# Performance work log

Hardware: AMD Instinct MI355X
Metric: run time of the kernel (lower is better)

Reference implementation:

```python
import jax, jax.numpy as jnp
import numpy as np

TEMP = 0.07
LAMBDA_INFONCE = 1.0
LAMBDA_NTXENT = 0.5
EPS = 1e-8

B, S, H, C = 32, 2048, 1024, 5


def _l2norm(x):
    # F.normalize-style row L2 normalization
    n = jnp.sqrt(jnp.sum(x * x, axis=1, keepdims=True))
    return x / jnp.maximum(n, 1e-12)


def _proj(x, W1, b1, W2, b2):
    h = jax.nn.relu(x @ W1 + b1)
    return _l2norm(h @ W2 + b2)


def setup_inputs() -> dict:
    key = jax.random.key(0)
    ks = jax.random.split(key, 12)
    sc1 = 1.0 / np.sqrt(H)
    sc2 = 1.0 / np.sqrt(H // 2)
    sc3 = 1.0 / np.sqrt(2 * H)
    return {
        "span_features": jax.random.normal(ks[0], (B, S, H), jnp.float32),
        "aspect_logits": jax.random.normal(ks[1], (B, S, C), jnp.float32),
        "opinion_logits": jax.random.normal(ks[2], (B, S, C), jnp.float32),
        "sentiment_labels": jax.random.randint(ks[3], (B,), 0, 3),
        "Wa1": jax.random.normal(ks[4], (H, H // 2), jnp.float32) * sc1,
        "ba1": jnp.zeros((H // 2,), jnp.float32),
        "Wa2": jax.random.normal(ks[5], (H // 2, 128), jnp.float32) * sc2,
        "ba2": jnp.zeros((128,), jnp.float32),
        "Wo1": jax.random.normal(ks[6], (H, H // 2), jnp.float32) * sc1,
        "bo1": jnp.zeros((H // 2,), jnp.float32),
        "Wo2": jax.random.normal(ks[7], (H // 2, 128), jnp.float32) * sc2,
        "bo2": jnp.zeros((128,), jnp.float32),
        "Ws1": jax.random.normal(ks[8], (2 * H, H), jnp.float32) * sc3,
        "bs1": jnp.zeros((H,), jnp.float32),
        "Ws2": jax.random.normal(ks[9], (H, 256), jnp.float32) * sc1,
        "bs2": jnp.zeros((256,), jnp.float32),
    }


def _pool(span_features, logits):
    # attention pooling: softmax over seq of summed non-O class logits
    w = jax.nn.softmax(logits[:, :, 1:].sum(axis=-1), axis=-1)  # [B, S]
    return jnp.einsum("bsh,bs->bh", span_features, w)  # [B, H]


def _infonce(a, o, labels):
    n = a.shape[0]
    sim = (a @ o.T) / TEMP  # [B, B]
    same = labels[:, None] == labels[None, :]
    eye = jnp.eye(n, dtype=a.dtype)
    pos_mask = eye + 0.5 * (same & (eye == 0)).astype(a.dtype)
    exp_sim = jnp.exp(sim)
    return -jnp.mean(jnp.log((exp_sim * pos_mask).sum(1) / exp_sim.sum(1) + EPS))


def _ntxent(s, labels):
    n = s.shape[0]
    s = _l2norm(s)
    sim = (s @ s.T) / TEMP
    same = (labels[:, None] == labels[None, :]).astype(s.dtype)
    mask = same - jnp.eye(n, dtype=s.dtype)
    exp_sim = jnp.exp(sim)
    pos = (exp_sim * mask).sum(1)
    neg = (exp_sim * (1.0 - mask)).sum(1)
    pos_count = mask.sum(1)
    has_pos = pos_count > 0
    row = jnp.where(has_pos,
                    -jnp.log(pos / (pos + neg) + EPS) / jnp.maximum(pos_count, 1.0),
                    0.0)
    return row.sum() / jnp.maximum(has_pos.sum(), 1).astype(s.dtype)


def reference(span_features, aspect_logits, opinion_logits, sentiment_labels,
              Wa1, ba1, Wa2, ba2, Wo1, bo1, Wo2, bo2, Ws1, bs1, Ws2, bs2):
    a_emb = _pool(span_features, aspect_logits)   # [B, H]
    o_emb = _pool(span_features, opinion_logits)  # [B, H]
    a_proj = _proj(a_emb, Wa1, ba1, Wa2, ba2)     # [B, 128]
    o_proj = _proj(o_emb, Wo1, bo1, Wo2, bo2)     # [B, 128]
    infonce = _infonce(a_proj, o_proj, sentiment_labels)
    s_proj = _proj(jnp.concatenate([a_emb, o_emb], axis=-1), Ws1, bs1, Ws2, bs2)
    ntxent = _ntxent(s_proj, sentiment_labels)
    # generation_embeddings is None -> cross_modal_loss = 0
    return LAMBDA_INFONCE * infonce + LAMBDA_NTXENT * ntxent
```

## Files before the change

kernel.cpp:

```cpp
#include <hip/hip_runtime.h>
#include <hip/hip_bf16.h>

#define BB 32
#define SS 2048
#define HH 1024
#define CC 5
#define TEMP_INV (1.0f/0.07f)

__global__ __launch_bounds__(256) void pool_weights(const float* __restrict__ alog,
                             const float* __restrict__ olog,
                             float* __restrict__ w_a,
                             float* __restrict__ w_o) {
    int b = blockIdx.x >> 1;
    int which = blockIdx.x & 1;
    const float* lg = which ? olog : alog;
    float* wout = which ? w_o : w_a;
    __shared__ float raw[SS * CC];
    __shared__ float sl[SS];
    __shared__ float red[256];
    int t = threadIdx.x;
    const float4* src = (const float4*)(lg + (size_t)b * SS * CC);
    float4* dst = (float4*)raw;
    #pragma unroll 4
    for (int i = t; i < SS * CC / 4; i += 256) dst[i] = src[i];
    __syncthreads();
    for (int s = t; s < SS; s += 256) {
        int base = s * 5;
        sl[s] = raw[base + 1] + raw[base + 2] + raw[base + 3] + raw[base + 4];
    }
    __syncthreads();
    float m = -1e30f;
    for (int s = t; s < SS; s += 256) m = fmaxf(m, sl[s]);
    red[t] = m;
    __syncthreads();
    for (int o = 128; o > 0; o >>= 1) {
        if (t < o) red[t] = fmaxf(red[t], red[t + o]);
        __syncthreads();
    }
    m = red[0];
    __syncthreads();
    float sum = 0.f;
    for (int s = t; s < SS; s += 256) {
        float e = expf(sl[s] - m);
        sl[s] = e;
        sum += e;
    }
    red[t] = sum;
    __syncthreads();
    for (int o = 128; o > 0; o >>= 1) {
        if (t < o) red[t] += red[t + o];
        __syncthreads();
    }
    float inv = 1.0f / red[0];
    for (int s = t; s < SS; s += 256) wout[(size_t)b * SS + s] = sl[s] * inv;
}

__global__ __launch_bounds__(256) void pool_partial(const float* __restrict__ span,
                             const float* __restrict__ w_a,
                             const float* __restrict__ w_o,
                             float* __restrict__ part_a,
                             float* __restrict__ part_o) {
    int b = blockIdx.x >> 5;
    int chunk = blockIdx.x & 31;
    int t = threadIdx.x;
    __shared__ float wa[64], wo[64];
    int s0 = chunk * 64;
    if (t < 64) {
        wa[t] = w_a[(size_t)b * SS + s0 + t];
        wo[t] = w_o[(size_t)b * SS + s0 + t];
    }
    __syncthreads();
    const float4* sp = (const float4*)span + ((size_t)b * SS + s0) * (HH / 4) + t;
    float4 aa = {0.f, 0.f, 0.f, 0.f};
    float4 oo = {0.f, 0.f, 0.f, 0.f};
    #pragma unroll 8
    for (int ss = 0; ss < 64; ++ss) {
        float4 v = sp[(size_t)ss * (HH / 4)];
        float fa = wa[ss], fo = wo[ss];
        aa.x += v.x * fa; aa.y += v.y * fa; aa.z += v.z * fa; aa.w += v.w * fa;
        oo.x += v.x * fo; oo.y += v.y * fo; oo.z += v.z * fo; oo.w += v.w * fo;
    }
    size_t idx = ((size_t)chunk * BB + b) * HH + (size_t)t * 4;
    *(float4*)(part_a + idx) = aa;
    *(float4*)(part_o + idx) = oo;
}

__global__ __launch_bounds__(256) void pool_reduce(const float* __restrict__ part_a,
                            const float* __restrict__ part_o,
                            float* __restrict__ a_emb,
                            float* __restrict__ o_emb) {
    int gid = blockIdx.x * 256 + threadIdx.x;
    int which = gid >> 15;
    int r = gid & 32767;
    const float* p = which ? part_o : part_a;
    float s = 0.f;
    #pragma unroll
    for (int c = 0; c < 32; ++c) s += p[(size_t)c * 32768 + r];
    (which ? o_emb : a_emb)[r] = s;
}

__global__ __launch_bounds__(512) void gemm1_all(const float* __restrict__ a_emb, const float* __restrict__ o_emb,
                          const float* __restrict__ Wa1, const float* __restrict__ Wo1,
                          const float* __restrict__ Ws1,
                          float* __restrict__ p1_a, float* __restrict__ p1_o,
                          float* __restrict__ p1_s) {
    int bid = blockIdx.x;
    const float* xp; const float* W; float* part; int N, kb, jb;
    if (bid < 64) {
        jb = bid & 7; kb = bid >> 3; N = 512; W = Wa1; part = p1_a;
        xp = a_emb + kb * 128;
    } else if (bid < 128) {
        int r = bid - 64;
        jb = r & 7; kb = r >> 3; N = 512; W = Wo1; part = p1_o;
        xp = o_emb + kb * 128;
    } else {
        int r = bid - 128;
        jb = r & 15; kb = r >> 4; N = 1024; W = Ws1; part = p1_s;
        int kk0 = kb * 128;
        xp = (kk0 < 1024) ? (a_emb + kk0) : (o_emb + (kk0 - 1024));
    }
    int k0 = kb * 128;
    __shared__ float xs[32][128];
    int t = threadIdx.x;
    #pragma unroll
    for (int i = 0; i < 2; ++i) {
        int f = t + i * 512;
        int b = f >> 5;
        int kk = (f & 31) * 4;
        *(float4*)(&xs[b][kk]) = *(const float4*)(xp + (size_t)b * HH + kk);
    }
    __syncthreads();
    int jl = t & 63, bg = t >> 6;
    int j = jb * 64 + jl;
    float acc[4] = {0.f, 0.f, 0.f, 0.f};
    const float* Wp = W + (size_t)k0 * N + j;
    #pragma unroll 4
    for (int k = 0; k < 128; k += 4) {
        float w0 = Wp[(size_t)(k + 0) * N];
        float w1 = Wp[(size_t)(k + 1) * N];
        float w2 = Wp[(size_t)(k + 2) * N];
        float w3 = Wp[(size_t)(k + 3) * N];
        #pragma unroll
        for (int bi = 0; bi < 4; ++bi) {
            float4 xv = *(const float4*)(&xs[bg * 4 + bi][k]);
            acc[bi] += xv.x * w0 + xv.y * w1 + xv.z * w2 + xv.w * w3;
        }
    }
    float* pp = part + (size_t)kb * 32 * N + j;
    #pragma unroll
    for (int bi = 0; bi < 4; ++bi)
        pp[(size_t)(bg * 4 + bi) * N] = acc[bi];
}

__global__ __launch_bounds__(512) void layer2_all(const float* __restrict__ p1_a, const float* __restrict__ ba1,
                           const float* __restrict__ Wa2, const float* __restrict__ ba2,
                           const float* __restrict__ p1_o, const float* __restrict__ bo1,
                           const float* __restrict__ Wo2, const float* __restrict__ bo2,
                           const float* __restrict__ p1_s, const float* __restrict__ bs1,
                           const float* __restrict__ Ws2, const float* __restrict__ bs2,
                           float* __restrict__ a_proj, float* __restrict__ o_proj,
                           float* __restrict__ s_proj) {
    __shared__ float x[1024];
    __shared__ float red[512];
    int bid = blockIdx.x;
    int t = threadIdx.x;
    if (bid < 64) {
        int which = bid >> 5;
        int b = bid & 31;
        const float* part = which ? p1_o : p1_a;
        const float* b1 = which ? bo1 : ba1;
        const float* W2 = which ? Wo2 : Wa2;
        const float* b2 = which ? bo2 : ba2;
        float* out = (which ? o_proj : a_proj) + (size_t)b * 128;
        {
            float s = b1[t];
            #pragma unroll
            for (int kb = 0; kb < 8; ++kb) s += part[(size_t)kb * 32 * 512 + (size_t)b * 512 + t];
            x[t] = fmaxf(s, 0.f);
        }
        __syncthreads();
        int jj = t & 127, kh = t >> 7;
        int kbase = kh * 128;
        const float* Wc = W2 + (size_t)kbase * 128 + jj;
        float acc = 0.f;
        #pragma unroll 16
        for (int kk = 0; kk < 128; ++kk)
            acc += x[kbase + kk] * Wc[(size_t)kk * 128];
        if (kh == 0) acc += b2[jj];
        red[t] = acc;
        __syncthreads();
        float tot = 0.f;
        if (t < 128) tot = red[t] + red[t + 128] + red[t + 256] + red[t + 384];
        __syncthreads();
        if (t < 128) red[t] = tot * tot;
        __syncthreads();
        for (int o = 64; o > 0; o >>= 1) {
            if (t < o) red[t] += red[t + o];
            __syncthreads();
        }
        float n = fmaxf(sqrtf(red[0]), 1e-12f);
        if (t < 128) out[t] = tot / n;
    } else {
        int b = bid - 64;
        for (int j = t; j < 1024; j += 512) {
            float s = bs1[j];
            #pragma unroll
            for (int kb = 0; kb < 16; ++kb) s += p1_s[(size_t)kb * 32 * 1024 + (size_t)b * 1024 + j];
            x[j] = fmaxf(s, 0.f);
        }
        __syncthreads();
        int jj = t & 255, kh = t >> 8;
        int kbase = kh * 512;
        const float* Wc = Ws2 + (size_t)kbase * 256 + jj;
        float acc = 0.f;
        #pragma unroll 16
        for (int kk = 0; kk < 512; ++kk)
            acc += x[kbase + kk] * Wc[(size_t)kk * 256];
        if (kh == 0) acc += bs2[jj];
        red[t] = acc;
        __syncthreads();
        float tot = 0.f;
        if (t < 256) tot = red[t] + red[t + 256];
        __syncthreads();
        if (t < 256) red[t] = tot * tot;
        __syncthreads();
        for (int o = 128; o > 0; o >>= 1) {
            if (t < o) red[t] += red[t + o];
            __syncthreads();
        }
        float n = fmaxf(sqrtf(red[0]), 1e-12f);
        if (t < 256) s_proj[(size_t)b * 256 + t] = tot / n;
    }
}

__global__ __launch_bounds__(1024) void loss_kernel(const float* __restrict__ a_proj,
                            const float* __restrict__ o_proj,
                            const float* __restrict__ s_proj,
                            const int* __restrict__ labels,
                            float* __restrict__ out) {
    __shared__ float ap[BB][129];
    __shared__ float op[BB][129];
    __shared__ float sp[BB][257];
    __shared__ float rowv[BB], rownt[BB];
    __shared__ int hp[BB], lab[BB];
    int t = threadIdx.x;
    for (int idx = t; idx < BB * 128; idx += 1024) {
        int r = idx >> 7, c = idx & 127;
        ap[r][c] = a_proj[idx];
        op[r][c] = o_proj[idx];
    }
    for (int idx = t; idx < BB * 256; idx += 1024) {
        int r = idx >> 8, c = idx & 255;
        sp[r][c] = s_proj[idx];
    }
    if (t < BB) lab[t] = labels[t];
    __syncthreads();
    int i = t >> 5, j = t & 31;

    float ssq = 0.f;
    #pragma unroll
    for (int k = 0; k < 8; ++k) {
        float v = sp[i][j * 8 + k];
        ssq += v * v;
    }
    for (int m = 16; m > 0; m >>= 1) ssq += __shfl_xor(ssq, m, 64);
    float inv = 1.0f / fmaxf(sqrtf(ssq), 1e-12f);
    for (int k = j; k < 256; k += 32) sp[i][k] *= inv;
    __syncthreads();

    float dot = 0.f;
    #pragma unroll 16
    for (int k = 0; k < 128; ++k) dot += ap[i][k] * op[j][k];
    float e = expf(dot * TEMP_INV);
    float maskv = (i == j) ? 1.0f : ((lab[i] == lab[j]) ? 0.5f : 0.0f);
    float num = e * maskv, den = e;
    for (int m = 16; m > 0; m >>= 1) {
        num += __shfl_xor(num, m, 64);
        den += __shfl_xor(den, m, 64);
    }

    float dn = 0.f;
    #pragma unroll 16
    for (int k = 0; k < 256; ++k) dn += sp[i][k] * sp[j][k];
    float en = expf(dn * TEMP_INV);
    float mnt = (lab[i] == lab[j]) ? ((i == j) ? 0.f : 1.f) : 0.f;
    float pos = en * mnt, neg = en * (1.f - mnt), pc = mnt;
    for (int m = 16; m > 0; m >>= 1) {
        pos += __shfl_xor(pos, m, 64);
        neg += __shfl_xor(neg, m, 64);
        pc += __shfl_xor(pc, m, 64);
    }

    if (j == 0) {
        rowv[i] = -logf(num / den + 1e-8f);
        bool has = pc > 0.f;
        rownt[i] = has ? (-logf(pos / (pos + neg) + 1e-8f) / fmaxf(pc, 1.0f)) : 0.f;
        hp[i] = has ? 1 : 0;
    }
    __syncthreads();
    if (t == 0) {
        float inf = 0.f, nt = 0.f;
        int h = 0;
        for (int q = 0; q < BB; ++q) { inf += rowv[q]; nt += rownt[q]; h += hp[q]; }
        inf /= (float)BB;
        nt /= (float)(h > 0 ? h : 1);
        out[0] = 1.0f * inf + 0.5f * nt;
    }
}

extern "C" void kernel_launch(void* const* d_in, const int* in_sizes, int n_in,
                              void* d_out, int out_size, void* d_ws, size_t ws_size,
                              hipStream_t stream) {
    const float* span  = (const float*)d_in[0];
    const float* alog  = (const float*)d_in[1];
    const float* olog  = (const float*)d_in[2];
    const int*   labs  = (const int*)d_in[3];
    const float* Wa1   = (const float*)d_in[4];
    const float* ba1   = (const float*)d_in[5];
    const float* Wa2   = (const float*)d_in[6];
    const float* ba2   = (const float*)d_in[7];
    const float* Wo1   = (const float*)d_in[8];
    const float* bo1   = (const float*)d_in[9];
    const float* Wo2   = (const float*)d_in[10];
    const float* bo2   = (const float*)d_in[11];
    const float* Ws1   = (const float*)d_in[12];
    const float* bs1   = (const float*)d_in[13];
    const float* Ws2   = (const float*)d_in[14];
    const float* bs2   = (const float*)d_in[15];

    float* ws = (float*)d_ws;
    float* w_a    = ws;
    float* w_o    = ws + 65536;
    float* part_a = ws + 131072;
    float* part_o = ws + 1179648;
    float* a_emb  = ws + 2228224;
    float* o_emb  = ws + 2260992;
    float* p1_a   = ws + 2293760;
    float* p1_o   = ws + 2424832;
    float* p1_s   = ws + 2555904;
    float* a_proj = ws + 3080192;
    float* o_proj = ws + 3084288;
    float* s_proj = ws + 3088384;

    hipLaunchKernelGGL(pool_weights, dim3(64), dim3(256), 0, stream, alog, olog, w_a, w_o);
    hipLaunchKernelGGL(pool_partial, dim3(1024), dim3(256), 0, stream,
                       span, w_a, w_o, part_a, part_o);
    hipLaunchKernelGGL(pool_reduce, dim3(256), dim3(256), 0, stream,
                       part_a, part_o, a_emb, o_emb);
    hipLaunchKernelGGL(gemm1_all, dim3(384), dim3(512), 0, stream,
                       a_emb, o_emb, Wa1, Wo1, Ws1, p1_a, p1_o, p1_s);
    hipLaunchKernelGGL(layer2_all, dim3(96), dim3(512), 0, stream,
                       p1_a, ba1, Wa2, ba2, p1_o, bo1, Wo2, bo2,
                       p1_s, bs1, Ws2, bs2, a_proj, o_proj, s_proj);
    hipLaunchKernelGGL(loss_kernel, dim3(1), dim3(1024), 0, stream,
                       a_proj, o_proj, s_proj, labs, (float*)d_out);
}
```

Baseline: 456.1 us.

## Split loss into per-row blocks plus final reduce; raise unroll factors

The single-block loss kernel becomes a 32-block kernel, one block per row. It uses float4 shared-memory loads and 8-lane shuffle reductions for the dot products, then a tiny second kernel sums the per-row terms. Unroll factors in pool_partial and gemm1_all are also raised. This spreads the serial loss work across CUs, at the cost of one more kernel launch and redundant loading and normalization of s_proj in every block.

Result: no change. 447.7 us (-1.8%).

```diff
diff --git a/kernel.cpp b/kernel.cpp
--- a/kernel.cpp
+++ b/kernel.cpp
@@ -73,7 +73,7 @@
     const float4* sp = (const float4*)span + ((size_t)b * SS + s0) * (HH / 4) + t;
     float4 aa = {0.f, 0.f, 0.f, 0.f};
     float4 oo = {0.f, 0.f, 0.f, 0.f};
-    #pragma unroll 8
+    #pragma unroll 16
     for (int ss = 0; ss < 64; ++ss) {
         float4 v = sp[(size_t)ss * (HH / 4)];
         float fa = wa[ss], fo = wo[ss];
@@ -134,7 +134,7 @@
     int j = jb * 64 + jl;
     float acc[4] = {0.f, 0.f, 0.f, 0.f};
     const float* Wp = W + (size_t)k0 * N + j;
-    #pragma unroll 4
+    #pragma unroll 8
     for (int k = 0; k < 128; k += 4) {
         float w0 = Wp[(size_t)(k + 0) * N];
         float w1 = Wp[(size_t)(k + 1) * N];
@@ -233,75 +233,118 @@
     }
 }
 
-__global__ __launch_bounds__(1024) void loss_kernel(const float* __restrict__ a_proj,
+__global__ __launch_bounds__(256) void loss_rows(const float* __restrict__ a_proj,
                             const float* __restrict__ o_proj,
                             const float* __restrict__ s_proj,
                             const int* __restrict__ labels,
-                            float* __restrict__ out) {
-    __shared__ float ap[BB][129];
-    __shared__ float op[BB][129];
-    __shared__ float sp[BB][257];
-    __shared__ float rowv[BB], rownt[BB];
-    __shared__ int hp[BB], lab[BB];
+                            float* __restrict__ rowbuf) {
+    int i = blockIdx.x;
+    __shared__ __align__(16) float spn[BB][260];
+    __shared__ __align__(16) float opn[BB][132];
+    __shared__ __align__(16) float api[128];
+    __shared__ float invn[BB];
+    __shared__ float jv[BB][5];
+    __shared__ int lab[BB];
     int t = threadIdx.x;
-    for (int idx = t; idx < BB * 128; idx += 1024) {
-        int r = idx >> 7, c = idx & 127;
-        ap[r][c] = a_proj[idx];
-        op[r][c] = o_proj[idx];
-    }
-    for (int idx = t; idx < BB * 256; idx += 1024) {
-        int r = idx >> 8, c = idx & 255;
-        sp[r][c] = s_proj[idx];
-    }
+    for (int q = t; q < 2048; q += 256) {
+        int r = q >> 6, c = (q & 63) << 2;
+        *(float4*)&spn[r][c] = *(const float4*)(s_proj + r * 256 + c);
+    }
+    for (int q = t; q < 1024; q += 256) {
+        int r = q >> 5, c = (q & 31) << 2;
+        *(float4*)&opn[r][c] = *(const float4*)(o_proj + r * 128 + c);
+    }
+    if (t < 32) *(float4*)&api[t * 4] = *(const float4*)(a_proj + (size_t)i * 128 + t * 4);
     if (t < BB) lab[t] = labels[t];
     __syncthreads();
-    int i = t >> 5, j = t & 31;
-
-    float ssq = 0.f;
+
+    int r = t >> 3, l = t & 7;
+    {
+        float ssq = 0.f;
+        #pragma unroll
+        for (int q = 0; q < 8; ++q) {
+            int c = (q * 8 + l) * 4;
+            float4 v = *(float4*)&spn[r][c];
+            ssq += v.x * v.x + v.y * v.y + v.z * v.z + v.w * v.w;
+        }
+        ssq += __shfl_xor(ssq, 1, 8);
+        ssq += __shfl_xor(ssq, 2, 8);
+        ssq += __shfl_xor(ssq, 4, 8);
+        if (l == 0) invn[r] = 1.0f / fmaxf(sqrtf(ssq), 1e-12f);
+    }
+    __syncthreads();
+    {
+        float s = invn[r];
+        #pragma unroll
+        for (int q = 0; q < 8; ++q) {
+            int c = (q * 8 + l) * 4;
+            float4 v = *(float4*)&spn[r][c];
+            v.x *= s; v.y *= s; v.z *= s; v.w *= s;
+            *(float4*)&spn[r][c] = v;
+        }
+    }
+    __syncthreads();
+
+    int j = r;
+    float dot = 0.f;
     #pragma unroll
-    for (int k = 0; k < 8; ++k) {
-        float v = sp[i][j * 8 + k];
-        ssq += v * v;
-    }
-    for (int m = 16; m > 0; m >>= 1) ssq += __shfl_xor(ssq, m, 64);
-    float inv = 1.0f / fmaxf(sqrtf(ssq), 1e-12f);
-    for (int k = j; k < 256; k += 32) sp[i][k] *= inv;
-    __syncthreads();
-
-    float dot = 0.f;
-    #pragma unroll 16
-    for (int k = 0; k < 128; ++k) dot += ap[i][k] * op[j][k];
-    float e = expf(dot * TEMP_INV);
-    float maskv = (i == j) ? 1.0f : ((lab[i] == lab[j]) ? 0.5f : 0.0f);
-    float num = e * maskv, den = e;
-    for (int m = 16; m > 0; m >>= 1) {
-        num += __shfl_xor(num, m, 64);
-        den += __shfl_xor(den, m, 64);
-    }
-
+    for (int q = 0; q < 4; ++q) {
+        int c = (q * 8 + l) * 4;
+        float4 av = *(float4*)&api[c];
+        float4 ov = *(float4*)&opn[j][c];
+        dot += av.x * ov.x + av.y * ov.y + av.z * ov.z + av.w * ov.w;
+    }
     float dn = 0.f;
-    #pragma unroll 16
-    for (int k = 0; k < 256; ++k) dn += sp[i][k] * sp[j][k];
-    float en = expf(dn * TEMP_INV);
-    float mnt = (lab[i] == lab[j]) ? ((i == j) ? 0.f : 1.f) : 0.f;
-    float pos = en * mnt, neg = en * (1.f - mnt), pc = mnt;
-    for (int m = 16; m > 0; m >>= 1) {
-        pos += __shfl_xor(pos, m, 64);
-        neg += __shfl_xor(neg, m, 64);
-        pc += __shfl_xor(pc, m, 64);
-    }
-
-    if (j == 0) {
-        rowv[i] = -logf(num / den + 1e-8f);
-        bool has = pc > 0.f;
-        rownt[i] = has ? (-logf(pos / (pos + neg) + 1e-8f) / fmaxf(pc, 1.0f)) : 0.f;
-        hp[i] = has ? 1 : 0;
-    }
-    __syncthreads();
-    if (t == 0) {
+    #pragma unroll
+    for (int q = 0; q < 8; ++q) {
+        int c = (q * 8 + l) * 4;
+        float4 si = *(float4*)&spn[i][c];
+        float4 sj = *(float4*)&spn[j][c];
+        dn += si.x * sj.x + si.y * sj.y + si.z * sj.z + si.w * sj.w;
+    }
+    dot += __shfl_xor(dot, 1, 8); dot += __shfl_xor(dot, 2, 8); dot += __shfl_xor(dot, 4, 8);
+    dn  += __shfl_xor(dn, 1, 8);  dn  += __shfl_xor(dn, 2, 8);  dn  += __shfl_xor(dn, 4, 8);
+    if (l == 0) {
+        float e = expf(dot * TEMP_INV);
+        float maskv = (i == j) ? 1.0f : ((lab[i] == lab[j]) ? 0.5f : 0.0f);
+        float en = expf(dn * TEMP_INV);
+        float mnt = (lab[i] == lab[j]) ? ((i == j) ? 0.f : 1.f) : 0.f;
+        jv[j][0] = e * maskv;
+        jv[j][1] = e;
+        jv[j][2] = en * mnt;
+        jv[j][3] = en * (1.f - mnt);
+        jv[j][4] = mnt;
+    }
+    __syncthreads();
+    if (t < 32) {
+        float num = jv[t][0], den = jv[t][1], pos = jv[t][2], neg = jv[t][3], pc = jv[t][4];
+        for (int m = 16; m > 0; m >>= 1) {
+            num += __shfl_xor(num, m, 32);
+            den += __shfl_xor(den, m, 32);
+            pos += __shfl_xor(pos, m, 32);
+            neg += __shfl_xor(neg, m, 32);
+            pc  += __shfl_xor(pc, m, 32);
+        }
+        if (t == 0) {
+            rowbuf[i] = -logf(num / den + 1e-8f);
+            bool has = pc > 0.f;
+            rowbuf[32 + i] = has ? (-logf(pos / (pos + neg) + 1e-8f) / fmaxf(pc, 1.0f)) : 0.f;
+            rowbuf[64 + i] = has ? 1.f : 0.f;
+        }
+    }
+}
+
+__global__ __launch_bounds__(64) void loss_final(const float* __restrict__ rowbuf,
+                                                 float* __restrict__ out) {
+    if (threadIdx.x == 0) {
         float inf = 0.f, nt = 0.f;
         int h = 0;
-        for (int q = 0; q < BB; ++q) { inf += rowv[q]; nt += rownt[q]; h += hp[q]; }
+        #pragma unroll
+        for (int q = 0; q < 32; ++q) {
+            inf += rowbuf[q];
+            nt += rowbuf[32 + q];
+            h += (rowbuf[64 + q] > 0.5f) ? 1 : 0;
+        }
         inf /= (float)BB;
         nt /= (float)(h > 0 ? h : 1);
         out[0] = 1.0f * inf + 0.5f * nt;
@@ -341,6 +384,7 @@
     float* a_proj = ws + 3080192;
     float* o_proj = ws + 3084288;
     float* s_proj = ws + 3088384;
+    float* rowbuf = ws + 3096576;
 
     hipLaunchKernelGGL(pool_weights, dim3(64), dim3(256), 0, stream, alog, olog, w_a, w_o);
     hipLaunchKernelGGL(pool_partial, dim3(1024), dim3(256), 0, stream,
@@ -352,6 +396,8 @@
     hipLaunchKernelGGL(layer2_all, dim3(96), dim3(512), 0, stream,
                        p1_a, ba1, Wa2, ba2, p1_o, bo1, Wo2, bo2,
                        p1_s, bs1, Ws2, bs2, a_proj, o_proj, s_proj);
-    hipLaunchKernelGGL(loss_kernel, dim3(1), dim3(1024), 0, stream,
-                       a_proj, o_proj, s_proj, labs, (float*)d_out);
-}
+    hipLaunchKernelGGL(loss_rows, dim3(32), dim3(256), 0, stream,
+                       a_proj, o_proj, s_proj, labs, rowbuf);
+    hipLaunchKernelGGL(loss_final, dim3(1), dim3(64), 0, stream,
+                       rowbuf, (float*)d_out);
+}
```
